# Performance work log

Hardware: AMD Instinct MI355X
Metric: run time of the kernel (lower is better)

Reference implementation:

```python
import jax, jax.numpy as jnp
import numpy as np

DT = 1.0
COLL_COEF = 0.5  # module in training mode
TWO_PI = 2.0 * np.pi


def safe_norm_ch(d):
    # L2 norm over channel axis (axis=1) with torch-like zero-safe gradient
    sq = jnp.sum(d * d, axis=1)
    nz = sq > 0
    return jnp.sqrt(jnp.where(nz, sq, 1.0)) * nz


def setup_inputs() -> dict:
    key = jax.random.key(0)
    k1, k2, k3, k4 = jax.random.split(key, 4)
    bs, C, X = 4, 256, 1024
    kinet_dim = 128
    n = kinet_dim  # n_divide = max_channal // C = 1
    P = n * (n - 1) // 2  # 8128
    return {
        "x": jax.random.normal(k1, (bs, C, X), jnp.float32),
        "v": jax.random.normal(k2, (bs, C, X), jnp.float32),
        "a": jax.random.normal(k3, (bs, C, X), jnp.float32),
        "rand_u": jax.random.uniform(k4, (bs, C, P), jnp.float32),
        "collision_dims": jnp.arange(kinet_dim, dtype=jnp.int32),
    }


def reference(x, v, a, rand_u, collision_dims):
    dims = collision_dims
    xs = x[:, :, dims]          # (bs, chnl, n)  (n_divide == 1, view is a no-op)
    as_ = a[:, :, dims]
    bs, chnl, n = xs.shape
    vv = as_ * DT               # code overwrites v with a*dt
    xx = xs

    # pairwise relative / center-of-mass quantities
    x_r = safe_norm_ch(xx[:, :, :, None] - xx[:, :, None, :])       # (bs, n, n)
    v_r = safe_norm_ch(vv[:, :, :, None] - vv[:, :, None, :])       # (bs, n, n)
    v_cm = (vv[:, :, :, None] + vv[:, :, None, :]) * 0.5            # (bs, chnl, n, n)
    x_cm = (xx[:, :, :, None] + xx[:, :, None, :]) * 0.5            # (bs, chnl, n, n)

    u_x = jnp.exp(-x_r)
    v_r_max = jnp.max(v_r, axis=(1, 2), keepdims=True)              # (bs, 1, 1)
    mask = v_r / v_r_max * u_x
    collision_mask = mask > (1.0 - COLL_COEF)                       # (bs, n, n) bool

    # antisymmetric projection of the upper triangle of v_r
    iu, ju = np.triu_indices(n, k=1)
    rand_vec = TWO_PI * rand_u                                      # (bs, chnl, P)
    proj = v_r[:, iu, ju][:, None, :] * rand_vec                    # (bs, chnl, P)
    vrl = jnp.zeros((bs, chnl, n, n), xs.dtype)
    vrl = vrl.at[:, :, iu, ju].set(proj)
    vrl = vrl.at[:, :, ju, iu].set(-proj)

    delta_v = v_cm + vrl - vv[:, :, :, None]                        # (bs, chnl, n, n)
    cmask = collision_mask[:, None, :, :]
    v_new = vv + jnp.sum(delta_v * cmask, axis=2)                   # (bs, chnl, n)

    cm = collision_mask.astype(xs.dtype) + jnp.eye(n, dtype=xs.dtype)[None]
    x_new = jnp.sum(x_cm * cm[:, None], axis=2) / jnp.sum(cm, axis=2)[:, None, :]
    x_new = x_new + v_new * (DT / 2.0)

    # reassemble: zero collision dims of x and a, add, write back updated coords
    out = x.at[:, :, dims].set(0.0) + a.at[:, :, dims].set(0.0)
    out = out.at[:, :, dims].set(x_new.reshape(bs, chnl, n))
    return out
```

## Files before the change

### kernel.cpp

```cpp
#include <hip/hip_runtime.h>
#include <math.h>

#define BS 4
#define CH 256
#define XD 1024
#define N 128
#define NP 8128
#define NTILE 36
#define NPASS 112
#define TWO_PI_F 6.283185307179586f
#define PADU 132

typedef __fp16 h2v __attribute__((ext_vector_type(2)));

__device__ __forceinline__ h2v u2h(unsigned u) {
  union { unsigned u; h2v h; } x; x.u = u; return x.h;
}
__device__ __forceinline__ unsigned h2u(h2v h) {
  union { unsigned u; h2v h; } x; x.h = h; return x.u;
}

__global__ __launch_bounds__(256) void k1_pair_pass(
    const float* __restrict__ x, const float* __restrict__ a,
    const int* __restrict__ dims,
    float* __restrict__ vrS, float* __restrict__ mS,
    float* __restrict__ pmaxV, float* __restrict__ pmaxM,
    float* __restrict__ out) {
  int bid = blockIdx.x;
  int t = threadIdx.x;
  __shared__ unsigned sXi[16][PADU], sXj[16][PADU], sAi[16][PADU], sAj[16][PADU];
  __shared__ unsigned inset[XD / 32];
  __shared__ float wred[16];

  if (bid < BS * NTILE) {
    int b = bid / NTILE, tt = bid % NTILE;
    int ti = 0;
    while (8 * (ti + 1) - ((ti + 1) * ti) / 2 <= tt) ++ti;
    int tj = ti + tt - (8 * ti - (ti * (ti - 1)) / 2);

    int d16 = t & 15, grp = t >> 4;
    int di = dims[ti * 16 + d16];
    int dj = dims[tj * 16 + d16];
    const float* xb = x + (size_t)b * CH * XD;
    const float* ab = a + (size_t)b * CH * XD;
    int c0 = grp * 16;
#pragma unroll
    for (int s = 0; s < 4; ++s) {
      const float* src = (s & 1) ? ab : xb;
      int d = (s & 2) ? dj : di;
      unsigned pk[8];
#pragma unroll
      for (int k = 0; k < 8; ++k) {
        float f0 = src[(size_t)(c0 + 2 * k) * XD + d];
        float f1 = src[(size_t)(c0 + 2 * k + 1) * XD + d];
        pk[k] = h2u(__builtin_amdgcn_cvt_pkrtz(f0, f1));
      }
      unsigned* dst = (s & 2) ? ((s & 1) ? &sAj[d16][0] : &sXj[d16][0])
                              : ((s & 1) ? &sAi[d16][0] : &sXi[d16][0]);
      *(uint4*)&dst[grp * 8] = make_uint4(pk[0], pk[1], pk[2], pk[3]);
      *(uint4*)&dst[grp * 8 + 4] = make_uint4(pk[4], pk[5], pk[6], pk[7]);
    }
    __syncthreads();

    int ii = t >> 4, jj = t & 15;
    float accx = 0.f, accv = 0.f;
#pragma unroll 8
    for (int cq = 0; cq < 32; ++cq) {
      uint4 xi = *(const uint4*)&sXi[ii][cq * 4];
      uint4 xj = *(const uint4*)&sXj[jj][cq * 4];
      uint4 ai = *(const uint4*)&sAi[ii][cq * 4];
      uint4 aj = *(const uint4*)&sAj[jj][cq * 4];
      h2v d0 = u2h(xi.x) - u2h(xj.x);
      accx = __builtin_amdgcn_fdot2(d0, d0, accx, false);
      h2v d1 = u2h(xi.y) - u2h(xj.y);
      accx = __builtin_amdgcn_fdot2(d1, d1, accx, false);
      h2v d2 = u2h(xi.z) - u2h(xj.z);
      accx = __builtin_amdgcn_fdot2(d2, d2, accx, false);
      h2v d3 = u2h(xi.w) - u2h(xj.w);
      accx = __builtin_amdgcn_fdot2(d3, d3, accx, false);
      h2v e0 = u2h(ai.x) - u2h(aj.x);
      accv = __builtin_amdgcn_fdot2(e0, e0, accv, false);
      h2v e1 = u2h(ai.y) - u2h(aj.y);
      accv = __builtin_amdgcn_fdot2(e1, e1, accv, false);
      h2v e2 = u2h(ai.z) - u2h(aj.z);
      accv = __builtin_amdgcn_fdot2(e2, e2, accv, false);
      h2v e3 = u2h(ai.w) - u2h(aj.w);
      accv = __builtin_amdgcn_fdot2(e3, e3, accv, false);
    }
    float vr = sqrtf(accv);
    float mv = vr * expf(-sqrtf(accx));
    int i = ti * 16 + ii, j = tj * 16 + jj;
    vrS[((size_t)b * N + i) * N + j] = vr;
    mS[((size_t)b * N + i) * N + j] = mv;

    float wv = vr, wm = mv;
#pragma unroll
    for (int off = 32; off; off >>= 1) {
      wv = fmaxf(wv, __shfl_xor(wv, off));
      wm = fmaxf(wm, __shfl_xor(wm, off));
    }
    int wid = t >> 6;
    if ((t & 63) == 0) { wred[wid] = wv; wred[8 + wid] = wm; }
    __syncthreads();
    if (t == 0) {
      pmaxV[b * NTILE + tt] = fmaxf(fmaxf(wred[0], wred[1]), fmaxf(wred[2], wred[3]));
      pmaxM[b * NTILE + tt] = fmaxf(fmaxf(wred[8], wred[9]), fmaxf(wred[10], wred[11]));
    }
  } else {
    int pb = bid - BS * NTILE;
    if (t < XD / 32) inset[t] = 0u;
    __syncthreads();
    if (t < N) atomicOr(&inset[dims[t] >> 5], 1u << (dims[t] & 31));
    __syncthreads();
    int r0 = (pb * (BS * CH)) / NPASS;
    int r1 = ((pb + 1) * (BS * CH)) / NPASS;
    for (int row = r0; row < r1; ++row) {
      const float4* x4 = (const float4*)(x + (size_t)row * XD);
      const float4* a4 = (const float4*)(a + (size_t)row * XD);
      float4* o4 = (float4*)(out + (size_t)row * XD);
      int e = t;
      unsigned nib = (inset[e >> 3] >> ((e & 7) * 4)) & 0xFu;
      float4 xv = x4[e], av = a4[e];
      float4 o;
      o.x = fmaf((nib & 1u) ? 0.5f : 1.0f, av.x, xv.x);
      o.y = fmaf((nib & 2u) ? 0.5f : 1.0f, av.y, xv.y);
      o.z = fmaf((nib & 4u) ? 0.5f : 1.0f, av.z, xv.z);
      o.w = fmaf((nib & 8u) ? 0.5f : 1.0f, av.w, xv.w);
      o4[e] = o;
    }
  }
}

__global__ __launch_bounds__(256) void k2_fixup(
    const float* __restrict__ x, const float* __restrict__ a,
    const float* __restrict__ ru, const int* __restrict__ dims,
    const float* __restrict__ vrS, const float* __restrict__ mS,
    const float* __restrict__ pmaxV, const float* __restrict__ pmaxM,
    float* __restrict__ out) {
  int cg = blockIdx.x, b = blockIdx.y;
  int t = threadIdx.x;
  __shared__ float mx2[2];
  __shared__ float xx[N], vv[N];
  __shared__ int dsh[N];

  if (t < 64) {
    float pv = (t < NTILE) ? pmaxV[b * NTILE + t] : 0.f;
    float pm = (t < NTILE) ? pmaxM[b * NTILE + t] : 0.f;
#pragma unroll
    for (int off = 32; off; off >>= 1) {
      pv = fmaxf(pv, __shfl_xor(pv, off));
      pm = fmaxf(pm, __shfl_xor(pm, off));
    }
    if (t == 0) { mx2[0] = pv; mx2[1] = pm; }
  }
  __syncthreads();
  float vrmax = mx2[0], mmax = mx2[1];
  float inv = vrmax > 0.f ? 1.f / vrmax : 0.f;
  if (!(mmax * inv > 0.5f)) return;

  if (t < N) dsh[t] = dims[t];
  for (int cc = 0; cc < 32; ++cc) {
    int c = (cg << 5) + cc;
    int bc = (b << 8) + c;
    __syncthreads();
    if (t < N) {
      int d = dsh[t];
      xx[t] = x[(size_t)bc * XD + d];
      vv[t] = a[(size_t)bc * XD + d];
    }
    __syncthreads();
    if (t < N) {
      int j = t;
      const float* rub = ru + (size_t)bc * NP;
      float S = 0.f, sumV = 0.f, sumX = 0.f, R = 0.f;
      for (int i = 0; i < N; ++i) {
        int lo = i < j ? i : j, hi = i < j ? j : i;
        size_t idx = ((size_t)b * N + lo) * N + hi;
        float mvv = mS[idx];
        if (mvv * inv > 0.5f) {
          S += 1.f;
          sumV += vv[i];
          sumX += xx[i];
          float vrv = vrS[idx];
          int p;
          float sgn;
          if (i < j) {
            p = i * N - ((i * (i + 1)) >> 1) + (j - i - 1);
            sgn = 1.f;
          } else {
            p = j * N - ((j * (j + 1)) >> 1) + (i - j - 1);
            sgn = -1.f;
          }
          R += sgn * TWO_PI_F * vrv * rub[p];
        }
      }
      float vj = vv[j];
      float v_new = vj + 0.5f * S * vj - 0.5f * sumV + R;
      float x_new = 0.5f * xx[j] + 0.5f * (xx[j] + sumX) / (S + 1.f) + 0.5f * v_new;
      out[(size_t)bc * XD + dsh[j]] = x_new;
    }
  }
}

extern "C" void kernel_launch(void* const* d_in, const int* in_sizes, int n_in,
                              void* d_out, int out_size, void* d_ws, size_t ws_size,
                              hipStream_t stream) {
  const float* x = (const float*)d_in[0];
  const float* a = (const float*)d_in[2];
  const float* ru = (const float*)d_in[3];
  const int* dims = (const int*)d_in[4];
  float* out = (float*)d_out;

  float* vrS = (float*)d_ws;
  float* mS = vrS + (size_t)BS * N * N;
  float* pmaxV = mS + (size_t)BS * N * N;
  float* pmaxM = pmaxV + BS * NTILE;

  k1_pair_pass<<<BS * NTILE + NPASS, 256, 0, stream>>>(x, a, dims, vrS, mS,
                                                       pmaxV, pmaxM, out);
  k2_fixup<<<dim3(8, BS), 256, 0, stream>>>(x, a, ru, dims, vrS, mS, pmaxV,
                                            pmaxM, out);
}
```

Measured before the change: 11.85 us.

## Merge passthrough into all blocks and vectorize tile loads for contiguous dims

```diff
diff --git a/kernel.cpp b/kernel.cpp
--- a/kernel.cpp
+++ b/kernel.cpp
@@ -7,7 +7,6 @@
 #define N 128
 #define NP 8128
 #define NTILE 36
-#define NPASS 112
 #define TWO_PI_F 6.283185307179586f
 #define PADU 132
 
@@ -31,90 +30,23 @@
   __shared__ unsigned sXi[16][PADU], sXj[16][PADU], sAi[16][PADU], sAj[16][PADU];
   __shared__ unsigned inset[XD / 32];
   __shared__ float wred[16];
-
-  if (bid < BS * NTILE) {
-    int b = bid / NTILE, tt = bid % NTILE;
-    int ti = 0;
-    while (8 * (ti + 1) - ((ti + 1) * ti) / 2 <= tt) ++ti;
-    int tj = ti + tt - (8 * ti - (ti * (ti - 1)) / 2);
-
-    int d16 = t & 15, grp = t >> 4;
-    int di = dims[ti * 16 + d16];
-    int dj = dims[tj * 16 + d16];
-    const float* xb = x + (size_t)b * CH * XD;
-    const float* ab = a + (size_t)b * CH * XD;
-    int c0 = grp * 16;
-#pragma unroll
-    for (int s = 0; s < 4; ++s) {
-      const float* src = (s & 1) ? ab : xb;
-      int d = (s & 2) ? dj : di;
-      unsigned pk[8];
-#pragma unroll
-      for (int k = 0; k < 8; ++k) {
-        float f0 = src[(size_t)(c0 + 2 * k) * XD + d];
-        float f1 = src[(size_t)(c0 + 2 * k + 1) * XD + d];
-        pk[k] = h2u(__builtin_amdgcn_cvt_pkrtz(f0, f1));
-      }
-      unsigned* dst = (s & 2) ? ((s & 1) ? &sAj[d16][0] : &sXj[d16][0])
-                              : ((s & 1) ? &sAi[d16][0] : &sXi[d16][0]);
-      *(uint4*)&dst[grp * 8] = make_uint4(pk[0], pk[1], pk[2], pk[3]);
-      *(uint4*)&dst[grp * 8 + 4] = make_uint4(pk[4], pk[5], pk[6], pk[7]);
-    }
-    __syncthreads();
-
-    int ii = t >> 4, jj = t & 15;
-    float accx = 0.f, accv = 0.f;
-#pragma unroll 8
-    for (int cq = 0; cq < 32; ++cq) {
-      uint4 xi = *(const uint4*)&sXi[ii][cq * 4];
-      uint4 xj = *(const uint4*)&sXj[jj][cq * 4];
-      uint4 ai = *(const uint4*)&sAi[ii][cq * 4];
-      uint4 aj = *(const uint4*)&sAj[jj][cq * 4];
-      h2v d0 = u2h(xi.x) - u2h(xj.x);
-      accx = __builtin_amdgcn_fdot2(d0, d0, accx, false);
-      h2v d1 = u2h(xi.y) - u2h(xj.y);
-      accx = __builtin_amdgcn_fdot2(d1, d1, accx, false);
-      h2v d2 = u2h(xi.z) - u2h(xj.z);
-      accx = __builtin_amdgcn_fdot2(d2, d2, accx, false);
-      h2v d3 = u2h(xi.w) - u2h(xj.w);
-      accx = __builtin_amdgcn_fdot2(d3, d3, accx, false);
-      h2v e0 = u2h(ai.x) - u2h(aj.x);
-      accv = __builtin_amdgcn_fdot2(e0, e0, accv, false);
-      h2v e1 = u2h(ai.y) - u2h(aj.y);
-      accv = __builtin_amdgcn_fdot2(e1, e1, accv, false);
-      h2v e2 = u2h(ai.z) - u2h(aj.z);
-      accv = __builtin_amdgcn_fdot2(e2, e2, accv, false);
-      h2v e3 = u2h(ai.w) - u2h(aj.w);
-      accv = __builtin_amdgcn_fdot2(e3, e3, accv, false);
-    }
-    float vr = sqrtf(accv);
-    float mv = vr * expf(-sqrtf(accx));
-    int i = ti * 16 + ii, j = tj * 16 + jj;
-    vrS[((size_t)b * N + i) * N + j] = vr;
-    mS[((size_t)b * N + i) * N + j] = mv;
-
-    float wv = vr, wm = mv;
-#pragma unroll
-    for (int off = 32; off; off >>= 1) {
-      wv = fmaxf(wv, __shfl_xor(wv, off));
-      wm = fmaxf(wm, __shfl_xor(wm, off));
-    }
-    int wid = t >> 6;
-    if ((t & 63) == 0) { wred[wid] = wv; wred[8 + wid] = wm; }
-    __syncthreads();
-    if (t == 0) {
-      pmaxV[b * NTILE + tt] = fmaxf(fmaxf(wred[0], wred[1]), fmaxf(wred[2], wred[3]));
-      pmaxM[b * NTILE + tt] = fmaxf(fmaxf(wred[8], wred[9]), fmaxf(wred[10], wred[11]));
-    }
-  } else {
-    int pb = bid - BS * NTILE;
-    if (t < XD / 32) inset[t] = 0u;
-    __syncthreads();
-    if (t < N) atomicOr(&inset[dims[t] >> 5], 1u << (dims[t] & 31));
-    __syncthreads();
-    int r0 = (pb * (BS * CH)) / NPASS;
-    int r1 = ((pb + 1) * (BS * CH)) / NPASS;
-    for (int row = r0; row < r1; ++row) {
+  __shared__ int contig;
+
+  if (t == 0) contig = 1;
+  if (t < XD / 32) inset[t] = 0u;
+  __syncthreads();
+  if (t < N) {
+    int d = dims[t];
+    atomicOr(&inset[d >> 5], 1u << (d & 31));
+    if (d != t) atomicAnd(&contig, 0);
+  }
+  __syncthreads();
+
+  {
+    int row0 = bid << 2;
+#pragma unroll
+    for (int r = 0; r < 4; ++r) {
+      int row = row0 + r;
       const float4* x4 = (const float4*)(x + (size_t)row * XD);
       const float4* a4 = (const float4*)(a + (size_t)row * XD);
       float4* o4 = (float4*)(out + (size_t)row * XD);
@@ -128,6 +60,105 @@
       o.w = fmaf((nib & 8u) ? 0.5f : 1.0f, av.w, xv.w);
       o4[e] = o;
     }
+  }
+
+  if (bid >= BS * NTILE) return;
+
+  int b = bid / NTILE, tt = bid % NTILE;
+  int ti = 0;
+  while (8 * (ti + 1) - ((ti + 1) * ti) / 2 <= tt) ++ti;
+  int tj = ti + tt - (8 * ti - (ti * (ti - 1)) / 2);
+  const float* xb = x + (size_t)b * CH * XD;
+  const float* ab = a + (size_t)b * CH * XD;
+
+  if (contig) {
+    int dg = t & 3, cidx = t >> 2;
+#pragma unroll
+    for (int s = 0; s < 4; ++s) {
+      const float* src = (s & 1) ? ab : xb;
+      int d0 = ((s & 2) ? tj : ti) * 16 + 4 * dg;
+      unsigned(*dst)[PADU] = (s & 2) ? ((s & 1) ? sAj : sXj)
+                                     : ((s & 1) ? sAi : sXi);
+#pragma unroll
+      for (int it = 0; it < 2; ++it) {
+        int cp = cidx + (it << 6);
+        float4 fa = *(const float4*)&src[(size_t)(2 * cp) * XD + d0];
+        float4 fb = *(const float4*)&src[(size_t)(2 * cp + 1) * XD + d0];
+        const float* pa = (const float*)&fa;
+        const float* pb = (const float*)&fb;
+#pragma unroll
+        for (int r = 0; r < 4; ++r) {
+          dst[4 * dg + r][cp] = h2u(__builtin_amdgcn_cvt_pkrtz(pa[r], pb[r]));
+        }
+      }
+    }
+  } else {
+    int d16 = t & 15, grp = t >> 4;
+    int di = dims[ti * 16 + d16];
+    int dj = dims[tj * 16 + d16];
+    int c0 = grp * 16;
+#pragma unroll
+    for (int s = 0; s < 4; ++s) {
+      const float* src = (s & 1) ? ab : xb;
+      int d = (s & 2) ? dj : di;
+      unsigned pk[8];
+#pragma unroll
+      for (int k = 0; k < 8; ++k) {
+        float f0 = src[(size_t)(c0 + 2 * k) * XD + d];
+        float f1 = src[(size_t)(c0 + 2 * k + 1) * XD + d];
+        pk[k] = h2u(__builtin_amdgcn_cvt_pkrtz(f0, f1));
+      }
+      unsigned* dstp = (s & 2) ? ((s & 1) ? &sAj[d16][0] : &sXj[d16][0])
+                               : ((s & 1) ? &sAi[d16][0] : &sXi[d16][0]);
+      *(uint4*)&dstp[grp * 8] = make_uint4(pk[0], pk[1], pk[2], pk[3]);
+      *(uint4*)&dstp[grp * 8 + 4] = make_uint4(pk[4], pk[5], pk[6], pk[7]);
+    }
+  }
+  __syncthreads();
+
+  int ii = t >> 4, jj = t & 15;
+  float accx = 0.f, accv = 0.f;
+#pragma unroll 8
+  for (int cq = 0; cq < 32; ++cq) {
+    uint4 xi = *(const uint4*)&sXi[ii][cq * 4];
+    uint4 xj = *(const uint4*)&sXj[jj][cq * 4];
+    uint4 ai = *(const uint4*)&sAi[ii][cq * 4];
+    uint4 aj = *(const uint4*)&sAj[jj][cq * 4];
+    h2v d0 = u2h(xi.x) - u2h(xj.x);
+    accx = __builtin_amdgcn_fdot2(d0, d0, accx, false);
+    h2v d1 = u2h(xi.y) - u2h(xj.y);
+    accx = __builtin_amdgcn_fdot2(d1, d1, accx, false);
+    h2v d2 = u2h(xi.z) - u2h(xj.z);
+    accx = __builtin_amdgcn_fdot2(d2, d2, accx, false);
+    h2v d3 = u2h(xi.w) - u2h(xj.w);
+    accx = __builtin_amdgcn_fdot2(d3, d3, accx, false);
+    h2v e0 = u2h(ai.x) - u2h(aj.x);
+    accv = __builtin_amdgcn_fdot2(e0, e0, accv, false);
+    h2v e1 = u2h(ai.y) - u2h(aj.y);
+    accv = __builtin_amdgcn_fdot2(e1, e1, accv, false);
+    h2v e2 = u2h(ai.z) - u2h(aj.z);
+    accv = __builtin_amdgcn_fdot2(e2, e2, accv, false);
+    h2v e3 = u2h(ai.w) - u2h(aj.w);
+    accv = __builtin_amdgcn_fdot2(e3, e3, accv, false);
+  }
+  float vr = sqrtf(accv);
+  float mv = vr * expf(-sqrtf(accx));
+  int i = ti * 16 + ii, j = tj * 16 + jj;
+  vrS[((size_t)b * N + i) * N + j] = vr;
+  mS[((size_t)b * N + i) * N + j] = mv;
+
+  float wv = vr, wm = mv;
+#pragma unroll
+  for (int off = 32; off; off >>= 1) {
+    wv = fmaxf(wv, __shfl_xor(wv, off));
+    wm = fmaxf(wm, __shfl_xor(wm, off));
+  }
+  int wid = t >> 6;
+  if ((t & 63) == 0) { wred[wid] = wv; wred[8 + wid] = wm; }
+  __syncthreads();
+  if (t == 0) {
+    pmaxV[b * NTILE + tt] = fmaxf(fmaxf(wred[0], wred[1]), fmaxf(wred[2], wred[3]));
+    pmaxM[b * NTILE + tt] = fmaxf(fmaxf(wred[8], wred[9]), fmaxf(wred[10], wred[11]));
   }
 }
 
@@ -216,8 +247,7 @@
   float* pmaxV = mS + (size_t)BS * N * N;
   float* pmaxM = pmaxV + BS * NTILE;
 
-  k1_pair_pass<<<BS * NTILE + NPASS, 256, 0, stream>>>(x, a, dims, vrS, mS,
-                                                       pmaxV, pmaxM, out);
+  k1_pair_pass<<<256, 256, 0, stream>>>(x, a, dims, vrS, mS, pmaxV, pmaxM, out);
   k2_fixup<<<dim3(8, BS), 256, 0, stream>>>(x, a, ru, dims, vrS, mS, pmaxV,
                                             pmaxM, out);
 }
```

After: 12.92 us. 9.0% more time.
